# Performance work log

Hardware: AMD Instinct MI355X
Metric: run time of the kernel (lower is better)

The kernel has to match this reference:

```python
import jax, jax.numpy as jnp
import numpy as np

NUM_HEADS = 16


def rotate_half(x):
    half = x.shape[-1] // 2
    return jnp.concatenate([-x[..., half:], x[..., :half]], axis=-1)


def setup_inputs() -> dict:
    key = jax.random.key(0)
    k0, k1, k2 = jax.random.split(key, 3)
    S, DIM, H = 16384, 1280, NUM_HEADS
    D = DIM // H            # 80
    G, L = 16, 1024         # 16 images, 1024 patch tokens each (S = G*L)

    hidden_states = jax.random.normal(k0, (S, DIM), dtype=jnp.float32) * 0.02

    # RoPE tables over packed positions
    pos = jnp.arange(S, dtype=jnp.float32)
    inv_freq = 1.0 / (10000.0 ** (jnp.arange(0, D, 2, dtype=jnp.float32) / D))
    freqs = pos[:, None] * inv_freq[None, :]          # [S, D/2]
    emb = jnp.concatenate([freqs, freqs], axis=-1)    # [S, D]
    cos = jnp.cos(emb)
    sin = jnp.sin(emb)

    cu_seqlens = (jnp.arange(G + 1, dtype=jnp.int32) * L)

    w_qkv = jax.random.normal(k1, (DIM, 3 * DIM), dtype=jnp.float32) * 0.02
    b_qkv = jnp.zeros((3 * DIM,), dtype=jnp.float32)
    w_proj = jax.random.normal(k2, (DIM, DIM), dtype=jnp.float32) * 0.02
    b_proj = jnp.zeros((DIM,), dtype=jnp.float32)

    return {
        "hidden_states": hidden_states,
        "cos": cos,
        "sin": sin,
        "w_qkv": w_qkv,
        "b_qkv": b_qkv,
        "w_proj": w_proj,
        "b_proj": b_proj,
        "cu_seqlens": cu_seqlens,
    }


def reference(hidden_states, cos, sin, w_qkv, b_qkv, w_proj, b_proj, cu_seqlens):
    S, DIM = hidden_states.shape
    H = NUM_HEADS
    D = DIM // H
    G = cu_seqlens.shape[0] - 1   # equal-length segments
    L = S // G

    qkv = (hidden_states @ w_qkv + b_qkv).reshape(S, 3, H, D)
    q, k, v = qkv[:, 0], qkv[:, 1], qkv[:, 2]   # [S, H, D]

    # RoPE (computed in fp32 as in source)
    c = cos[:, None, :]
    s = sin[:, None, :]
    q = q * c + rotate_half(q) * s
    k = k * c + rotate_half(k) * s

    # Source applies head_dim**-0.5 on q AND SDPA's default head_dim**-0.5,
    # so effective scale is head_dim**-1.
    scale = 1.0 / D

    qg = q.reshape(G, L, H, D)
    kg = k.reshape(G, L, H, D)
    vg = v.reshape(G, L, H, D)

    scores = jnp.einsum('glhd,gmhd->ghlm', qg, kg) * scale  # [G,H,L,L]
    attn = jax.nn.softmax(scores, axis=-1)
    out = jnp.einsum('ghlm,gmhd->glhd', attn, vg)           # [G,L,H,D]
    out = out.reshape(S, H * D)
    return out @ w_proj + b_proj
```

## Files before the change

kernel.cpp:

```cpp
#include <hip/hip_runtime.h>
#include <cmath>

#define SEQ   16384
#define DIMV  1280
#define NH    16
#define HD    80
#define NG    16
#define GL    1024
#define LDQKV (3*DIMV)

typedef short s16x8 __attribute__((ext_vector_type(8)));
typedef float f32x4 __attribute__((ext_vector_type(4)));

__device__ __forceinline__ unsigned short f2bf(float f) {
    union { float f; unsigned int u; } v; v.f = f;
    unsigned int u = v.u;
    return (unsigned short)((u + 0x7FFFu + ((u >> 16) & 1u)) >> 16);
}
__device__ __forceinline__ float bf2f(unsigned short h) {
    union { unsigned int u; float f; } v; v.u = ((unsigned int)h) << 16;
    return v.f;
}
__device__ __forceinline__ unsigned int pack2(float a, float b) {
    return (unsigned int)f2bf(a) | ((unsigned int)f2bf(b) << 16);
}
__device__ __forceinline__ void gload_lds16(const void* g, void* l) {
    __builtin_amdgcn_global_load_lds(
        (const __attribute__((address_space(1))) unsigned int*)g,
        (__attribute__((address_space(3))) unsigned int*)l,
        16, 0, 0);
}

__global__ __launch_bounds__(256) void convert_bf16_kernel(
    const float* __restrict__ src, unsigned short* __restrict__ dst, int n)
{
    int i = (blockIdx.x * 256 + threadIdx.x) * 8;
    if (i >= n) return;
    float4 a = *(const float4*)&src[i];
    float4 b = *(const float4*)&src[i + 4];
    uint4 o;
    o.x = pack2(a.x, a.y); o.y = pack2(a.z, a.w);
    o.z = pack2(b.x, b.y); o.w = pack2(b.z, b.w);
    *(uint4*)&dst[i] = o;
}

__global__ __launch_bounds__(256) void transpose_bf16_kernel(
    const float* __restrict__ W, unsigned short* __restrict__ WT,
    int Kdim, int N)
{
    __shared__ float tile[32][33];
    const int bx = blockIdx.x * 32;
    const int by = blockIdx.y * 32;
    const int tx = threadIdx.x & 31, ty = threadIdx.x >> 5;
#pragma unroll
    for (int j = 0; j < 4; ++j)
        tile[ty + j * 8][tx] = W[(size_t)(by + ty + j * 8) * N + bx + tx];
    __syncthreads();
#pragma unroll
    for (int j = 0; j < 4; ++j)
        WT[(size_t)(bx + ty + j * 8) * Kdim + by + tx] =
            f2bf(tile[tx][ty + j * 8]);
}

template <bool BF16_OUT>
__global__ __launch_bounds__(256) void gemm_bf16_kernel(
    const unsigned short* __restrict__ A,
    const unsigned short* __restrict__ BT,
    const float* __restrict__ bias,
    void* __restrict__ C, int ldc, int K)
{
    __shared__ unsigned short As[128 * 64];
    __shared__ unsigned short Bs[128 * 64];
    const int t    = threadIdx.x;
    const int w    = t >> 6, lane = t & 63;
    const int wr   = w >> 1, wc = w & 1;
    const int gr   = lane >> 4, c15 = lane & 15;
    const int bm   = blockIdx.y * 128, bn = blockIdx.x * 128;

    f32x4 acc[4][4];
#pragma unroll
    for (int m = 0; m < 4; ++m)
#pragma unroll
        for (int n = 0; n < 4; ++n) acc[m][n] = (f32x4){0.f, 0.f, 0.f, 0.f};

    for (int kt = 0; kt < K; kt += 64) {
#pragma unroll
        for (int i = 0; i < 4; ++i) {
            int idx = t + i * 256;
            int row = idx >> 3;
            int cb  = ((idx & 7) ^ (row & 7)) << 4;
            gload_lds16((const char*)A + ((size_t)(bm + row) * K + kt) * 2 + cb,
                        (char*)As + idx * 16);
            gload_lds16((const char*)BT + ((size_t)(bn + row) * K + kt) * 2 + cb,
                        (char*)Bs + idx * 16);
        }
        __syncthreads();

#pragma unroll
        for (int ks = 0; ks < 2; ++ks) {
            s16x8 af[4], bf_[4];
#pragma unroll
            for (int m = 0; m < 4; ++m) {
                int row = wr * 64 + m * 16 + c15;
                int col = (ks * 64 + gr * 16) ^ ((row & 7) << 4);
                af[m] = *(const s16x8*)((const char*)As + row * 128 + col);
            }
#pragma unroll
            for (int n = 0; n < 4; ++n) {
                int row = wc * 64 + n * 16 + c15;
                int col = (ks * 64 + gr * 16) ^ ((row & 7) << 4);
                bf_[n] = *(const s16x8*)((const char*)Bs + row * 128 + col);
            }
#pragma unroll
            for (int m = 0; m < 4; ++m)
#pragma unroll
                for (int n = 0; n < 4; ++n)
                    acc[m][n] = __builtin_amdgcn_mfma_f32_16x16x32_bf16(
                        af[m], bf_[n], acc[m][n], 0, 0, 0);
        }
        __syncthreads();
    }

#pragma unroll
    for (int m = 0; m < 4; ++m) {
        int row0 = bm + wr * 64 + m * 16 + gr * 4;
#pragma unroll
        for (int n = 0; n < 4; ++n) {
            int col = bn + wc * 64 + n * 16 + c15;
            float bv = bias[col];
#pragma unroll
            for (int j = 0; j < 4; ++j) {
                float v = acc[m][n][j] + bv;
                if (BF16_OUT)
                    ((unsigned short*)C)[(size_t)(row0 + j) * ldc + col] = f2bf(v);
                else
                    ((float*)C)[(size_t)(row0 + j) * ldc + col] = v;
            }
        }
    }
}

__global__ __launch_bounds__(256) void rope_bf16_kernel(
    unsigned short* __restrict__ qkv,
    const float* __restrict__ cos_t,
    const float* __restrict__ sin_t)
{
    int u = blockIdx.x * 256 + threadIdx.x;
    if (u >= SEQ * NH * 20) return;
    int s   = u / (NH * 20);
    int rem = u % (NH * 20);
    int h   = rem / 20;
    int d   = (rem % 20) * 2;

    float2 c  = *(const float2*)&cos_t[s * HD + d];
    float2 sn = *(const float2*)&sin_t[s * HD + d];
    size_t base = (size_t)s * LDQKV + h * HD + d;

#pragma unroll
    for (int part = 0; part < 2; ++part) {
        size_t b = base + part * DIMV;
        unsigned int lo = *(unsigned int*)&qkv[b];
        unsigned int hi = *(unsigned int*)&qkv[b + 40];
        float x0 = bf2f((unsigned short)lo), x1 = bf2f((unsigned short)(lo >> 16));
        float y0 = bf2f((unsigned short)hi), y1 = bf2f((unsigned short)(hi >> 16));
        *(unsigned int*)&qkv[b]      = pack2(x0 * c.x - y0 * sn.x, x1 * c.y - y1 * sn.y);
        *(unsigned int*)&qkv[b + 40] = pack2(y0 * c.x + x0 * sn.x, y1 * c.y + x1 * sn.y);
    }
}

__global__ __launch_bounds__(512) void attn_mfma_kernel(
    const unsigned short* __restrict__ qkv,
    unsigned short* __restrict__ ao)
{
    const int bx = blockIdx.x;
    const int qt = bx & 7;
    const int h  = (bx >> 3) & 15;
    const int g  = bx >> 7;

    __shared__ unsigned short Ks[64][104];
    __shared__ unsigned short Vt[80][72];
    __shared__ unsigned short Pl[8][16][72];

    const int t    = threadIdx.x;
    const int w    = t >> 6;
    const int lane = t & 63;
    const int gr   = lane >> 4;
    const int c15  = lane & 15;

    const size_t qrow0 = (size_t)g * GL + (size_t)qt * 128;

    {
        int r = t >> 3, cp = t & 7;
        *(unsigned int*)&Ks[r][80 + cp * 2] = 0u;
    }

    s16x8 qf[3];
    {
        const unsigned short* qp = qkv + (qrow0 + w * 16 + c15) * LDQKV + h * HD;
#pragma unroll
        for (int kk = 0; kk < 3; ++kk) {
            int d0 = kk * 32 + gr * 8;
            if (d0 < 80) qf[kk] = *(const s16x8*)&qp[d0];
            else         qf[kk] = (s16x8){0,0,0,0,0,0,0,0};
        }
    }

    f32x4 oacc[5];
#pragma unroll
    for (int nt = 0; nt < 5; ++nt) oacc[nt] = (f32x4){0.f, 0.f, 0.f, 0.f};
    float mrow[4], lrow[4];
#pragma unroll
    for (int r = 0; r < 4; ++r) { mrow[r] = -1e30f; lrow[r] = 0.f; }

    const float scale = 1.0f / 80.0f;

    for (int kc = 0; kc < GL / 64; ++kc) {
        __syncthreads();

#pragma unroll
        for (int s = 0; s < 2; ++s) {
            int i = t + 512 * s;
            if (i < 640) {
                int r = i / 10, cc = i % 10;
                const unsigned short* src =
                    qkv + ((size_t)g * GL + kc * 64 + r) * LDQKV + DIMV + h * HD + cc * 8;
                *(uint4*)&Ks[r][cc * 8] = *(const uint4*)src;
            }
        }
#pragma unroll
        for (int s = 0; s < 2; ++s) {
            int i = t + 512 * s;
            if (i < 640) {
                int r = i & 63, c8 = i >> 6;
                const unsigned short* src =
                    qkv + ((size_t)g * GL + kc * 64 + r) * LDQKV + 2 * DIMV + h * HD + c8 * 8;
                uint4 x = *(const uint4*)src;
                Vt[c8 * 8 + 0][r] = (unsigned short)(x.x);
                Vt[c8 * 8 + 1][r] = (unsigned short)(x.x >> 16);
                Vt[c8 * 8 + 2][r] = (unsigned short)(x.y);
                Vt[c8 * 8 + 3][r] = (unsigned short)(x.y >> 16);
                Vt[c8 * 8 + 4][r] = (unsigned short)(x.z);
                Vt[c8 * 8 + 5][r] = (unsigned short)(x.z >> 16);
                Vt[c8 * 8 + 6][r] = (unsigned short)(x.w);
                Vt[c8 * 8 + 7][r] = (unsigned short)(x.w >> 16);
            }
        }
        __syncthreads();

        f32x4 sacc[4];
#pragma unroll
        for (int nt = 0; nt < 4; ++nt) {
            f32x4 a = (f32x4){0.f, 0.f, 0.f, 0.f};
#pragma unroll
            for (int kk = 0; kk < 3; ++kk) {
                s16x8 kfrag = *(const s16x8*)&Ks[nt * 16 + c15][kk * 32 + gr * 8];
                a = __builtin_amdgcn_mfma_f32_16x16x32_bf16(qf[kk], kfrag, a, 0, 0, 0);
            }
            sacc[nt] = a * scale;
        }

        float rmax[4];
#pragma unroll
        for (int r = 0; r < 4; ++r)
            rmax[r] = fmaxf(fmaxf(sacc[0][r], sacc[1][r]),
                            fmaxf(sacc[2][r], sacc[3][r]));
#pragma unroll
        for (int m = 1; m < 16; m <<= 1)
#pragma unroll
            for (int r = 0; r < 4; ++r)
                rmax[r] = fmaxf(rmax[r], __shfl_xor(rmax[r], m, 64));
        float alpha[4];
#pragma unroll
        for (int r = 0; r < 4; ++r) {
            float mnew = fmaxf(mrow[r], rmax[r]);
            alpha[r] = __expf(mrow[r] - mnew);
            mrow[r] = mnew;
        }
        float rsum[4] = {0.f, 0.f, 0.f, 0.f};
#pragma unroll
        for (int nt = 0; nt < 4; ++nt)
#pragma unroll
            for (int r = 0; r < 4; ++r) {
                float p = __expf(sacc[nt][r] - mrow[r]);
                sacc[nt][r] = p;
                rsum[r] += p;
            }
#pragma unroll
        for (int m = 1; m < 16; m <<= 1)
#pragma unroll
            for (int r = 0; r < 4; ++r)
                rsum[r] += __shfl_xor(rsum[r], m, 64);
#pragma unroll
        for (int r = 0; r < 4; ++r)
            lrow[r] = lrow[r] * alpha[r] + rsum[r];
#pragma unroll
        for (int nt = 0; nt < 5; ++nt)
#pragma unroll
            for (int r = 0; r < 4; ++r)
                oacc[nt][r] *= alpha[r];

#pragma unroll
        for (int nt = 0; nt < 4; ++nt)
#pragma unroll
            for (int r = 0; r < 4; ++r)
                Pl[w][gr * 4 + r][nt * 16 + c15] = f2bf(sacc[nt][r]);
        asm volatile("s_waitcnt lgkmcnt(0)" ::: "memory");
        __builtin_amdgcn_sched_barrier(0);
        s16x8 pa[2];
        pa[0] = *(const s16x8*)&Pl[w][c15][gr * 8];
        pa[1] = *(const s16x8*)&Pl[w][c15][32 + gr * 8];

#pragma unroll
        for (int nt = 0; nt < 5; ++nt) {
            f32x4 o = oacc[nt];
#pragma unroll
            for (int kk2 = 0; kk2 < 2; ++kk2) {
                s16x8 vfrag = *(const s16x8*)&Vt[nt * 16 + c15][kk2 * 32 + gr * 8];
                o = __builtin_amdgcn_mfma_f32_16x16x32_bf16(pa[kk2], vfrag, o, 0, 0, 0);
            }
            oacc[nt] = o;
        }
    }

    float inv[4];
#pragma unroll
    for (int r = 0; r < 4; ++r) inv[r] = 1.0f / lrow[r];
    const size_t orow0 = qrow0 + w * 16;
#pragma unroll
    for (int nt = 0; nt < 5; ++nt)
#pragma unroll
        for (int r = 0; r < 4; ++r)
            ao[(orow0 + gr * 4 + r) * DIMV + h * HD + nt * 16 + c15] =
                f2bf(oacc[nt][r] * inv[r]);
}

extern "C" void kernel_launch(void* const* d_in, const int* in_sizes, int n_in,
                              void* d_out, int out_size, void* d_ws, size_t ws_size,
                              hipStream_t stream)
{
    const float* hidden = (const float*)d_in[0];
    const float* cos_t  = (const float*)d_in[1];
    const float* sin_t  = (const float*)d_in[2];
    const float* w_qkv  = (const float*)d_in[3];
    const float* b_qkv  = (const float*)d_in[4];
    const float* w_proj = (const float*)d_in[5];
    const float* b_proj = (const float*)d_in[6];

    float* out = (float*)d_out;

    char* ws = (char*)d_ws;
    unsigned short* qkv_bf = (unsigned short*)(ws);
    unsigned short* hbf    = (unsigned short*)(ws + 125829120);
    unsigned short* ao_bf  = (unsigned short*)(ws + 167772160);
    unsigned short* wqkvT  = (unsigned short*)(ws + 209715200);
    unsigned short* wprojT = (unsigned short*)(ws + 219545600);

    {
        int n = SEQ * DIMV;
        convert_bf16_kernel<<<n / 8 / 256, 256, 0, stream>>>(hidden, hbf, n);
        transpose_bf16_kernel<<<dim3(3 * DIMV / 32, DIMV / 32), 256, 0, stream>>>(
            w_qkv, wqkvT, DIMV, 3 * DIMV);
        transpose_bf16_kernel<<<dim3(DIMV / 32, DIMV / 32), 256, 0, stream>>>(
            w_proj, wprojT, DIMV, DIMV);
    }
    gemm_bf16_kernel<true><<<dim3(3 * DIMV / 128, SEQ / 128), 256, 0, stream>>>(
        hbf, wqkvT, b_qkv, qkv_bf, 3 * DIMV, DIMV);
    {
        int n = SEQ * NH * 20;
        rope_bf16_kernel<<<n / 256, 256, 0, stream>>>(qkv_bf, cos_t, sin_t);
    }
    attn_mfma_kernel<<<dim3(NG * NH * (GL / 128)), 512, 0, stream>>>(qkv_bf, ao_bf);
    gemm_bf16_kernel<false><<<dim3(DIMV / 128, SEQ / 128), 256, 0, stream>>>(
        ao_bf, wprojT, b_proj, out, DIMV, DIMV);
}
```

Measured before the change: 756.1 us.

## Prefetch next K/V tile into registers and skip rescaling with lazy softmax max

The attention kernel now issues global loads for the next 64-row K/V chunk into registers right after the LDS barrier, so they overlap with the current chunk's MFMA and softmax work. The loop body then only stores registers into LDS. It also adds a lazy online-softmax update: the running max and the rescale of the accumulator and row sum happen only when some row's max rises by more than 8, decided across the warp. This removes most of the exp and multiply rescale work, at the cost of extra registers that may lower occupancy, and lets exponentials run against a stale max within a bounded range.

```diff
diff --git a/kernel.cpp b/kernel.cpp
--- a/kernel.cpp
+++ b/kernel.cpp
@@ -188,10 +188,35 @@
     const int c15  = lane & 15;
 
     const size_t qrow0 = (size_t)g * GL + (size_t)qt * 128;
+    const unsigned short* kvbase = qkv + (size_t)g * GL * LDQKV;
 
     {
         int r = t >> 3, cp = t & 7;
         *(unsigned int*)&Ks[r][80 + cp * 2] = 0u;
+    }
+
+    const int kr0_r = t / 10,         kr0_c = t % 10;
+    const int kr1_r = (t + 512) / 10, kr1_c = (t + 512) % 10;
+    const int vr_r  = t & 63;
+    const int vc0   = t >> 6;
+    const int vc1   = 8 + (t >> 6);
+    const bool two  = (t < 128);
+
+    const size_t offK0 = (size_t)kr0_r * LDQKV + DIMV + h * HD + kr0_c * 8;
+    const size_t offK1 = (size_t)kr1_r * LDQKV + DIMV + h * HD + kr1_c * 8;
+    const size_t offV0 = (size_t)vr_r  * LDQKV + 2 * DIMV + h * HD + vc0 * 8;
+    const size_t offV1 = (size_t)vr_r  * LDQKV + 2 * DIMV + h * HD + vc1 * 8;
+
+    uint4 kr0, kr1, vr0, vr1;
+
+    {
+        const unsigned short* base = kvbase;
+        kr0 = *(const uint4*)&base[offK0];
+        vr0 = *(const uint4*)&base[offV0];
+        if (two) {
+            kr1 = *(const uint4*)&base[offK1];
+            vr1 = *(const uint4*)&base[offV1];
+        }
     }
 
     s16x8 qf[3];
@@ -217,35 +242,41 @@
     for (int kc = 0; kc < GL / 64; ++kc) {
         __syncthreads();
 
-#pragma unroll
-        for (int s = 0; s < 2; ++s) {
-            int i = t + 512 * s;
-            if (i < 640) {
-                int r = i / 10, cc = i % 10;
-                const unsigned short* src =
-                    qkv + ((size_t)g * GL + kc * 64 + r) * LDQKV + DIMV + h * HD + cc * 8;
-                *(uint4*)&Ks[r][cc * 8] = *(const uint4*)src;
-            }
-        }
-#pragma unroll
-        for (int s = 0; s < 2; ++s) {
-            int i = t + 512 * s;
-            if (i < 640) {
-                int r = i & 63, c8 = i >> 6;
-                const unsigned short* src =
-                    qkv + ((size_t)g * GL + kc * 64 + r) * LDQKV + 2 * DIMV + h * HD + c8 * 8;
-                uint4 x = *(const uint4*)src;
-                Vt[c8 * 8 + 0][r] = (unsigned short)(x.x);
-                Vt[c8 * 8 + 1][r] = (unsigned short)(x.x >> 16);
-                Vt[c8 * 8 + 2][r] = (unsigned short)(x.y);
-                Vt[c8 * 8 + 3][r] = (unsigned short)(x.y >> 16);
-                Vt[c8 * 8 + 4][r] = (unsigned short)(x.z);
-                Vt[c8 * 8 + 5][r] = (unsigned short)(x.z >> 16);
-                Vt[c8 * 8 + 6][r] = (unsigned short)(x.w);
-                Vt[c8 * 8 + 7][r] = (unsigned short)(x.w >> 16);
-            }
+        *(uint4*)&Ks[kr0_r][kr0_c * 8] = kr0;
+        if (two) *(uint4*)&Ks[kr1_r][kr1_c * 8] = kr1;
+        {
+            uint4 x = vr0;
+            Vt[vc0 * 8 + 0][vr_r] = (unsigned short)(x.x);
+            Vt[vc0 * 8 + 1][vr_r] = (unsigned short)(x.x >> 16);
+            Vt[vc0 * 8 + 2][vr_r] = (unsigned short)(x.y);
+            Vt[vc0 * 8 + 3][vr_r] = (unsigned short)(x.y >> 16);
+            Vt[vc0 * 8 + 4][vr_r] = (unsigned short)(x.z);
+            Vt[vc0 * 8 + 5][vr_r] = (unsigned short)(x.z >> 16);
+            Vt[vc0 * 8 + 6][vr_r] = (unsigned short)(x.w);
+            Vt[vc0 * 8 + 7][vr_r] = (unsigned short)(x.w >> 16);
+        }
+        if (two) {
+            uint4 x = vr1;
+            Vt[vc1 * 8 + 0][vr_r] = (unsigned short)(x.x);
+            Vt[vc1 * 8 + 1][vr_r] = (unsigned short)(x.x >> 16);
+            Vt[vc1 * 8 + 2][vr_r] = (unsigned short)(x.y);
+            Vt[vc1 * 8 + 3][vr_r] = (unsigned short)(x.y >> 16);
+            Vt[vc1 * 8 + 4][vr_r] = (unsigned short)(x.z);
+            Vt[vc1 * 8 + 5][vr_r] = (unsigned short)(x.z >> 16);
+            Vt[vc1 * 8 + 6][vr_r] = (unsigned short)(x.w);
+            Vt[vc1 * 8 + 7][vr_r] = (unsigned short)(x.w >> 16);
         }
         __syncthreads();
+
+        if (kc + 1 < GL / 64) {
+            const unsigned short* base = kvbase + (size_t)(kc + 1) * 64 * LDQKV;
+            kr0 = *(const uint4*)&base[offK0];
+            vr0 = *(const uint4*)&base[offV0];
+            if (two) {
+                kr1 = *(const uint4*)&base[offK1];
+                vr1 = *(const uint4*)&base[offV1];
+            }
+        }
 
         f32x4 sacc[4];
 #pragma unroll
@@ -269,13 +300,27 @@
 #pragma unroll
             for (int r = 0; r < 4; ++r)
                 rmax[r] = fmaxf(rmax[r], __shfl_xor(rmax[r], m, 64));
-        float alpha[4];
-#pragma unroll
-        for (int r = 0; r < 4; ++r) {
-            float mnew = fmaxf(mrow[r], rmax[r]);
-            alpha[r] = __expf(mrow[r] - mnew);
-            mrow[r] = mnew;
-        }
+
+        bool need = false;
+#pragma unroll
+        for (int r = 0; r < 4; ++r)
+            need = need || (rmax[r] > mrow[r] + 8.0f);
+        if (__any(need)) {
+            float alpha[4];
+#pragma unroll
+            for (int r = 0; r < 4; ++r) {
+                float mnew = fmaxf(mrow[r], rmax[r]);
+                alpha[r] = __expf(mrow[r] - mnew);
+                mrow[r] = mnew;
+                lrow[r] *= alpha[r];
+            }
+#pragma unroll
+            for (int nt = 0; nt < 5; ++nt)
+#pragma unroll
+                for (int r = 0; r < 4; ++r)
+                    oacc[nt][r] *= alpha[r];
+        }
+
         float rsum[4] = {0.f, 0.f, 0.f, 0.f};
 #pragma unroll
         for (int nt = 0; nt < 4; ++nt)
@@ -292,12 +337,7 @@
                 rsum[r] += __shfl_xor(rsum[r], m, 64);
 #pragma unroll
         for (int r = 0; r < 4; ++r)
-            lrow[r] = lrow[r] * alpha[r] + rsum[r];
-#pragma unroll
-        for (int nt = 0; nt < 5; ++nt)
-#pragma unroll
-            for (int r = 0; r < 4; ++r)
-                oacc[nt][r] *= alpha[r];
+            lrow[r] += rsum[r];
 
 #pragma unroll
         for (int nt = 0; nt < 4; ++nt)
```

After: 740.9 us. 1.02x faster.
